# Performance work log

Measured on AMD Instinct MI355X. Metric: run time of the kernel, lower is better.

Reference implementation:

```python
import jax, jax.numpy as jnp
import numpy as np

H = 512
W = 512
SAMPLES = 32        # samples_per_segment hardcoded in render_filled_path
SIGMA = 1.0         # default anti-aliasing width
CHUNK = 32          # edges processed per scan step (mirrors torch chunk_size)


def setup_inputs() -> dict:
    key = jax.random.key(0)
    k1, k2 = jax.random.split(key)
    # 64 cubic segments -> 3*64+1 = 193 control points in image coordinates
    scale = jnp.array([W, H], dtype=jnp.float32)
    control_points = jax.random.uniform(k1, (193, 2), dtype=jnp.float32) * scale
    color = jax.random.uniform(k2, (3,), dtype=jnp.float32)
    return {"control_points": control_points, "color": color}


def _sample_bezier(cp):
    # cp: [3S+1, 2] -> sampled points [S*SAMPLES, 2]
    S = (cp.shape[0] - 1) // 3
    p0 = cp[0:3 * S:3][:, None, :]      # [S,1,2]
    p1 = cp[1:3 * S:3][:, None, :]
    p2 = cp[2:3 * S:3][:, None, :]
    p3 = cp[3:3 * S + 1:3][:, None, :]
    t = jnp.linspace(0.0, 1.0, SAMPLES, dtype=jnp.float32)[None, :, None]  # [1,T,1]
    mt = 1.0 - t
    pts = (mt ** 3) * p0 + 3.0 * (mt ** 2) * t * p1 + 3.0 * mt * (t ** 2) * p2 + (t ** 3) * p3
    return pts.reshape(-1, 2)  # [S*T, 2]


def _winding(path_points, sigma):
    # soft scanline winding number over HxW grid, edges (j, (j+1)%M)
    M = path_points.shape[0]
    p0 = path_points                      # [M,2]
    p1 = jnp.roll(path_points, -1, axis=0)
    gy = jnp.arange(H, dtype=jnp.float32)[:, None]   # [H,1]
    gx = jnp.arange(W, dtype=jnp.float32)[None, :]   # [1,W]
    # M = 64*32 = 2048 is divisible by CHUNK
    edges = jnp.stack([p0, p1], axis=1).reshape(M // CHUNK, CHUNK, 2, 2)

    def body(wind, ech):
        a, b = ech[:, 0], ech[:, 1]                       # [CHUNK,2]
        x0 = a[:, 0][:, None, None]; y0 = a[:, 1][:, None, None]
        x1 = b[:, 0][:, None, None]; y1 = b[:, 1][:, None, None]
        dy = y1 - y0                                      # [CHUNK,1,1]
        t_cross = (gy[None] - y0) / (dy + 1e-8)           # [CHUNK,H,1]
        x_cross = x0 + t_cross * (x1 - x0)                # [CHUNK,H,1]
        valid_t = jax.nn.sigmoid(t_cross * 20.0) * jax.nn.sigmoid((1.0 - t_cross) * 20.0)
        crosses = jax.nn.sigmoid((x_cross - gx[None]) / sigma)  # [CHUNK,H,W]
        mask = (jnp.abs(dy) >= 1e-6).astype(jnp.float32)  # skip degenerate edges
        contrib = crosses * (valid_t * jnp.sign(dy) * mask)
        return wind + jnp.sum(contrib, axis=0), None

    wind0 = jnp.zeros((H, W), dtype=jnp.float32)
    wind, _ = jax.lax.scan(body, wind0, edges)
    return wind


def reference(control_points, color):
    path = _sample_bezier(control_points)        # [2048,2]
    winding = _winding(path, SIGMA)              # [H,W]
    alpha = jax.nn.sigmoid(winding * 4.0)
    rgb = jnp.broadcast_to(color[None, None, :], (H, W, 3))
    return jnp.concatenate([rgb, alpha[..., None]], axis=-1)  # [H,W,4]
```

## Files before the change

### kernel.cpp

```cpp
#include <hip/hip_runtime.h>
#include <math.h>

#define HH 512
#define WW 512
#define M 2048
#define TPB 256
#define TWIN 18
#define WPIX 37
#define EPB 6

__device__ __forceinline__ float sigmoidf(float z) {
    return __builtin_amdgcn_rcpf(1.0f + __expf(-z));
}

__global__ __launch_bounds__(TPB) void bezier_render_kernel(
    const float* __restrict__ cp,
    const float* __restrict__ color,
    float* __restrict__ out)
{
    __shared__ float2 cps2[194];
    __shared__ float2 pts[M];
    __shared__ float  smoothv[WW];
    __shared__ float  cbin[WW + 1];
    __shared__ float  wtot[4];
    __shared__ float2 act[M];
    __shared__ int    nact;

    const int t    = threadIdx.x;
    const int lane = t & 63;
    const int wv   = t >> 6;
    const int y    = blockIdx.x;
    const float gy = (float)y;

    if (t < 193) cps2[t] = ((const float2*)cp)[t];
    if (t == 0) { nact = 0; cbin[WW] = 0.0f; }
    for (int x = t; x < WW; x += TPB) { smoothv[x] = 0.0f; cbin[x] = 0.0f; }
    __syncthreads();

    for (int m = t; m < M; m += TPB) {
        int s = m >> 5;
        int i = m & 31;
        float tt = (float)i * (1.0f / 31.0f);
        float mt = 1.0f - tt;
        float w0 = mt * mt * mt;
        float w1 = 3.0f * mt * mt * tt;
        float w2 = 3.0f * mt * tt * tt;
        float w3 = tt * tt * tt;
        float2 P0 = cps2[3 * s], P1 = cps2[3 * s + 1];
        float2 P2 = cps2[3 * s + 2], P3 = cps2[3 * s + 3];
        pts[m] = make_float2(w0 * P0.x + w1 * P1.x + w2 * P2.x + w3 * P3.x,
                             w0 * P0.y + w1 * P1.y + w2 * P2.y + w3 * P3.y);
    }
    __syncthreads();

    for (int e = t; e < M; e += TPB) {
        float2 a = pts[e];
        float2 b = pts[(e + 1) & (M - 1)];
        float dy = b.y - a.y;
        float tc = (gy - a.y) * __builtin_amdgcn_rcpf(dy + 1e-8f);
        if (!(fabsf(dy) >= 1e-6f) || !(tc > -0.8059f) || !(tc < 1.8059f)) continue;
        float ea = __expf(-20.0f * tc);
        float eb = __expf(-20.0f * (1.0f - tc));
        float v = __builtin_amdgcn_rcpf((1.0f + ea) * (1.0f + eb));
        float w = (dy > 0.0f) ? v : -v;
        float xc = fmaf(tc, b.x - a.x, a.x);
        int A = (int)floorf(xc) - TWIN;
        int bin = (A > WW) ? WW : A;
        if (bin > 0) atomicAdd(&cbin[bin], w);
        if (A < WW && A > -WPIX) {
            int idx = atomicAdd(&nact, 1);
            act[idx] = make_float2(xc, w);
        }
    }
    __syncthreads();

    {
        int na = nact;
        int el = t / WPIX;
        int k  = t - el * WPIX;
        if (el < EPB) {
            for (int e = el; e < na; e += EPB) {
                float2 xw = act[e];
                int x = (int)floorf(xw.x) - TWIN + k;
                if ((unsigned)x < (unsigned)WW) {
                    atomicAdd(&smoothv[x], xw.y * sigmoidf(xw.x - (float)x));
                }
            }
        }
    }
    __syncthreads();

    float e0 = cbin[2 * t];
    float e1 = cbin[2 * t + 1];
    float p  = e0 + e1;
    float v  = p;
#pragma unroll
    for (int off = 1; off < 64; off <<= 1) {
        float o = __shfl_down(v, off, 64);
        if (lane + off < 64) v += o;
    }
    if (lane == 0) wtot[wv] = v;
    __syncthreads();
    float hsum = 0.0f;
    if (wv < 1) hsum += wtot[1];
    if (wv < 2) hsum += wtot[2];
    if (wv < 3) hsum += wtot[3];
    float S    = v - p + hsum;
    float c512 = cbin[WW];
    float wc1  = S + c512;
    float wc0  = e1 + wc1;

    float r = color[0], g = color[1], bl = color[2];
    int x0 = 2 * t;
    float a0 = sigmoidf(4.0f * (wc0 + smoothv[x0]));
    float a1 = sigmoidf(4.0f * (wc1 + smoothv[x0 + 1]));
    float4* out4 = (float4*)out;
    out4[y * WW + x0]     = make_float4(r, g, bl, a0);
    out4[y * WW + x0 + 1] = make_float4(r, g, bl, a1);
}

extern "C" void kernel_launch(void* const* d_in, const int* in_sizes, int n_in,
                              void* d_out, int out_size, void* d_ws, size_t ws_size,
                              hipStream_t stream) {
    const float* cp    = (const float*)d_in[0];
    const float* color = (const float*)d_in[1];
    float* out = (float*)d_out;
    bezier_render_kernel<<<dim3(HH), dim3(TPB), 0, stream>>>(cp, color, out);
}
```

Measured before the change: 71.48 us.

## Bin edge crossings per row in a pre-pass instead of per-row full edge scan

Splits the single render kernel into three launches: a zeroing kernel, an edge-binning kernel and a render kernel. In the binning kernel one wavefront per edge computes the rows that edge can affect and appends (x-crossing, weight) records to per-row global lists using atomic counters. The render kernel then reads only its row's records instead of every block resampling the Bezier curve and testing all 2048 edges. The aim is to remove the redundant per-row sampling and edge tests. In exchange it adds two extra launches, global atomic traffic and a workspace round trip.

Result: slower. 77.78 us (+8.8%).

```diff
diff --git a/kernel.cpp b/kernel.cpp
--- a/kernel.cpp
+++ b/kernel.cpp
@@ -8,79 +8,114 @@
 #define TWIN 18
 #define WPIX 37
 #define EPB 6
+#define CAP 2048
+
 
 __device__ __forceinline__ float sigmoidf(float z) {
     return __builtin_amdgcn_rcpf(1.0f + __expf(-z));
 }
 
-__global__ __launch_bounds__(TPB) void bezier_render_kernel(
+__device__ __forceinline__ float2 sample_pt(const float2* __restrict__ cp2, int m) {
+    int s = m >> 5;
+    int i = m & 31;
+    float tt = (float)i * (1.0f / 31.0f);
+    float mt = 1.0f - tt;
+    float w0 = mt * mt * mt;
+    float w1 = 3.0f * mt * mt * tt;
+    float w2 = 3.0f * mt * tt * tt;
+    float w3 = tt * tt * tt;
+    float2 P0 = cp2[3 * s], P1 = cp2[3 * s + 1];
+    float2 P2 = cp2[3 * s + 2], P3 = cp2[3 * s + 3];
+    return make_float2(w0 * P0.x + w1 * P1.x + w2 * P2.x + w3 * P3.x,
+                       w0 * P0.y + w1 * P1.y + w2 * P2.y + w3 * P3.y);
+}
+
+__global__ __launch_bounds__(256) void zero_kernel(int* __restrict__ cnt) {
+    int t = threadIdx.x;
+    cnt[t] = 0;
+    cnt[t + 256] = 0;
+}
+
+__global__ __launch_bounds__(TPB) void bin_kernel(
     const float* __restrict__ cp,
-    const float* __restrict__ color,
+    int* __restrict__ cnt,
+    float2* __restrict__ rec)
+{
+    const int lane = threadIdx.x & 63;
+    const int e = (blockIdx.x << 2) + (threadIdx.x >> 6);
+
+    const float2* cp2 = (const float2*)cp;
+    float2 a = sample_pt(cp2, e);
+    float2 b = sample_pt(cp2, (e + 1) & (M - 1));
+
+    float dy = b.y - a.y;
+    if (!(fabsf(dy) >= 1e-6f)) return;
+
+    float d    = dy + 1e-8f;
+    float rcpd = __builtin_amdgcn_rcpf(d);
+
+    float g0 = fmaf(-0.8059f, d, a.y);
+    float g1 = fmaf( 1.8059f, d, a.y);
+    float lo = fminf(g0, g1), hi = fmaxf(g0, g1);
+    int r0 = (int)floorf(lo); if (r0 < 0)  r0 = 0;
+    int r1 = (int)ceilf(hi);  if (r1 > HH - 1) r1 = HH - 1;
+
+    float dx = b.x - a.x;
+    for (int r = r0 + lane; r <= r1; r += 64) {
+        float gy = (float)r;
+        float tc = (gy - a.y) * rcpd;
+        if (!(tc > -0.8059f) || !(tc < 1.8059f)) continue;
+        float ea = __expf(-20.0f * tc);
+        float eb = __expf(-20.0f * (1.0f - tc));
+        float v  = __builtin_amdgcn_rcpf((1.0f + ea) * (1.0f + eb));
+        float w  = (dy > 0.0f) ? v : -v;
+        float xc = fmaf(tc, dx, a.x);
+        int A = (int)floorf(xc) - TWIN;
+        if (A > -WPIX) {
+            int idx = atomicAdd(&cnt[r], 1);
+            if (idx < CAP) rec[(r << 11) + idx] = make_float2(xc, w);
+        }
+    }
+}
+
+__global__ __launch_bounds__(TPB) void render_kernel(
+    const int*    __restrict__ cnt,
+    const float2* __restrict__ rec,
+    const float*  __restrict__ color,
     float* __restrict__ out)
 {
-    __shared__ float2 cps2[194];
-    __shared__ float2 pts[M];
+    __shared__ float2 act[CAP];
     __shared__ float  smoothv[WW];
     __shared__ float  cbin[WW + 1];
     __shared__ float  wtot[4];
-    __shared__ float2 act[M];
-    __shared__ int    nact;
 
     const int t    = threadIdx.x;
     const int lane = t & 63;
     const int wv   = t >> 6;
     const int y    = blockIdx.x;
-    const float gy = (float)y;
 
-    if (t < 193) cps2[t] = ((const float2*)cp)[t];
-    if (t == 0) { nact = 0; cbin[WW] = 0.0f; }
+    int na = cnt[y];
+    if (na > CAP) na = CAP;
+
     for (int x = t; x < WW; x += TPB) { smoothv[x] = 0.0f; cbin[x] = 0.0f; }
+    if (t == 0) cbin[WW] = 0.0f;
     __syncthreads();
 
-    for (int m = t; m < M; m += TPB) {
-        int s = m >> 5;
-        int i = m & 31;
-        float tt = (float)i * (1.0f / 31.0f);
-        float mt = 1.0f - tt;
-        float w0 = mt * mt * mt;
-        float w1 = 3.0f * mt * mt * tt;
-        float w2 = 3.0f * mt * tt * tt;
-        float w3 = tt * tt * tt;
-        float2 P0 = cps2[3 * s], P1 = cps2[3 * s + 1];
-        float2 P2 = cps2[3 * s + 2], P3 = cps2[3 * s + 3];
-        pts[m] = make_float2(w0 * P0.x + w1 * P1.x + w2 * P2.x + w3 * P3.x,
-                             w0 * P0.y + w1 * P1.y + w2 * P2.y + w3 * P3.y);
-    }
-    __syncthreads();
-
-    for (int e = t; e < M; e += TPB) {
-        float2 a = pts[e];
-        float2 b = pts[(e + 1) & (M - 1)];
-        float dy = b.y - a.y;
-        float tc = (gy - a.y) * __builtin_amdgcn_rcpf(dy + 1e-8f);
-        if (!(fabsf(dy) >= 1e-6f) || !(tc > -0.8059f) || !(tc < 1.8059f)) continue;
-        float ea = __expf(-20.0f * tc);
-        float eb = __expf(-20.0f * (1.0f - tc));
-        float v = __builtin_amdgcn_rcpf((1.0f + ea) * (1.0f + eb));
-        float w = (dy > 0.0f) ? v : -v;
-        float xc = fmaf(tc, b.x - a.x, a.x);
-        int A = (int)floorf(xc) - TWIN;
+    for (int e2 = t; e2 < na; e2 += TPB) {
+        float2 xw = rec[(y << 11) + e2];
+        act[e2] = xw;
+        int A = (int)floorf(xw.x) - TWIN;
         int bin = (A > WW) ? WW : A;
-        if (bin > 0) atomicAdd(&cbin[bin], w);
-        if (A < WW && A > -WPIX) {
-            int idx = atomicAdd(&nact, 1);
-            act[idx] = make_float2(xc, w);
-        }
+        if (bin > 0) atomicAdd(&cbin[bin], xw.y);
     }
     __syncthreads();
 
     {
-        int na = nact;
         int el = t / WPIX;
         int k  = t - el * WPIX;
         if (el < EPB) {
-            for (int e = el; e < na; e += EPB) {
-                float2 xw = act[e];
+            for (int e2 = el; e2 < na; e2 += EPB) {
+                float2 xw = act[e2];
                 int x = (int)floorf(xw.x) - TWIN + k;
                 if ((unsigned)x < (unsigned)WW) {
                     atomicAdd(&smoothv[x], xw.y * sigmoidf(xw.x - (float)x));
@@ -125,5 +160,11 @@
     const float* cp    = (const float*)d_in[0];
     const float* color = (const float*)d_in[1];
     float* out = (float*)d_out;
-    bezier_render_kernel<<<dim3(HH), dim3(TPB), 0, stream>>>(cp, color, out);
+
+    int*    cnt = (int*)d_ws;
+    float2* rec = (float2*)((char*)d_ws + 4096);
+
+    zero_kernel  <<<dim3(1),     dim3(256), 0, stream>>>(cnt);
+    bin_kernel   <<<dim3(M / 4), dim3(TPB), 0, stream>>>(cp, cnt, rec);
+    render_kernel<<<dim3(HH),    dim3(TPB), 0, stream>>>(cnt, rec, color, out);
 }
```

## Process two rows per block to share Bezier sampling and edge setup

Applied to the files above, without the earlier changes.

Each block now handles two image rows with 512 threads instead of one row with 256. The Bezier sampling into shared memory and the per-edge setup (dy, reciprocal, dx) are computed once and reused for both rows, halving the redundant per-block sampling work. The cost is doubling shared memory for the per-row buffers and halving the grid to 256 blocks, which on a 256-CU device may reduce latency hiding and occupancy.

After: 77.67 us. +8.7%, slower.

```diff
diff --git a/kernel.cpp b/kernel.cpp
--- a/kernel.cpp
+++ b/kernel.cpp
@@ -4,7 +4,8 @@
 #define HH 512
 #define WW 512
 #define M 2048
-#define TPB 256
+#define TPB 512
+#define ROWS 2
 #define TWIN 18
 #define WPIX 37
 #define EPB 6
@@ -20,21 +21,23 @@
 {
     __shared__ float2 cps2[194];
     __shared__ float2 pts[M];
-    __shared__ float  smoothv[WW];
-    __shared__ float  cbin[WW + 1];
-    __shared__ float  wtot[4];
-    __shared__ float2 act[M];
-    __shared__ int    nact;
+    __shared__ float  smoothv[ROWS][WW];
+    __shared__ float  cbin[ROWS][WW + 1];
+    __shared__ float  wtot[ROWS][4];
+    __shared__ float2 act[ROWS][M];
+    __shared__ int    nact[ROWS];
 
     const int t    = threadIdx.x;
     const int lane = t & 63;
-    const int wv   = t >> 6;
-    const int y    = blockIdx.x;
-    const float gy = (float)y;
+    const int grp  = t >> 8;
+    const int tl   = t & 255;
+    const int wv   = tl >> 6;
+    const int y0   = blockIdx.x * ROWS;
 
     if (t < 193) cps2[t] = ((const float2*)cp)[t];
-    if (t == 0) { nact = 0; cbin[WW] = 0.0f; }
-    for (int x = t; x < WW; x += TPB) { smoothv[x] = 0.0f; cbin[x] = 0.0f; }
+    if (t < ROWS) { nact[t] = 0; cbin[t][WW] = 0.0f; }
+    for (int x = t; x < ROWS * WW; x += TPB) smoothv[x >> 9][x & (WW - 1)] = 0.0f;
+    for (int x = t; x < ROWS * WW; x += TPB) cbin[x >> 9][x & (WW - 1)] = 0.0f;
     __syncthreads();
 
     for (int m = t; m < M; m += TPB) {
@@ -57,41 +60,48 @@
         float2 a = pts[e];
         float2 b = pts[(e + 1) & (M - 1)];
         float dy = b.y - a.y;
-        float tc = (gy - a.y) * __builtin_amdgcn_rcpf(dy + 1e-8f);
-        if (!(fabsf(dy) >= 1e-6f) || !(tc > -0.8059f) || !(tc < 1.8059f)) continue;
-        float ea = __expf(-20.0f * tc);
-        float eb = __expf(-20.0f * (1.0f - tc));
-        float v = __builtin_amdgcn_rcpf((1.0f + ea) * (1.0f + eb));
-        float w = (dy > 0.0f) ? v : -v;
-        float xc = fmaf(tc, b.x - a.x, a.x);
-        int A = (int)floorf(xc) - TWIN;
-        int bin = (A > WW) ? WW : A;
-        if (bin > 0) atomicAdd(&cbin[bin], w);
-        if (A < WW && A > -WPIX) {
-            int idx = atomicAdd(&nact, 1);
-            act[idx] = make_float2(xc, w);
+        if (!(fabsf(dy) >= 1e-6f)) continue;
+        float rcpd = __builtin_amdgcn_rcpf(dy + 1e-8f);
+        float dx = b.x - a.x;
+#pragma unroll
+        for (int rr = 0; rr < ROWS; ++rr) {
+            float gy = (float)(y0 + rr);
+            float tc = (gy - a.y) * rcpd;
+            if (!(tc > -0.8059f) || !(tc < 1.8059f)) continue;
+            float ea = __expf(-20.0f * tc);
+            float eb = __expf(-20.0f * (1.0f - tc));
+            float v = __builtin_amdgcn_rcpf((1.0f + ea) * (1.0f + eb));
+            float w = (dy > 0.0f) ? v : -v;
+            float xc = fmaf(tc, dx, a.x);
+            int A = (int)floorf(xc) - TWIN;
+            int bin = (A > WW) ? WW : A;
+            if (bin > 0) atomicAdd(&cbin[rr][bin], w);
+            if (A < WW && A > -WPIX) {
+                int idx = atomicAdd(&nact[rr], 1);
+                act[rr][idx] = make_float2(xc, w);
+            }
         }
     }
     __syncthreads();
 
     {
-        int na = nact;
-        int el = t / WPIX;
-        int k  = t - el * WPIX;
+        int na = nact[grp];
+        int el = tl / WPIX;
+        int k  = tl - el * WPIX;
         if (el < EPB) {
             for (int e = el; e < na; e += EPB) {
-                float2 xw = act[e];
+                float2 xw = act[grp][e];
                 int x = (int)floorf(xw.x) - TWIN + k;
                 if ((unsigned)x < (unsigned)WW) {
-                    atomicAdd(&smoothv[x], xw.y * sigmoidf(xw.x - (float)x));
+                    atomicAdd(&smoothv[grp][x], xw.y * sigmoidf(xw.x - (float)x));
                 }
             }
         }
     }
     __syncthreads();
 
-    float e0 = cbin[2 * t];
-    float e1 = cbin[2 * t + 1];
+    float e0 = cbin[grp][2 * tl];
+    float e1 = cbin[grp][2 * tl + 1];
     float p  = e0 + e1;
     float v  = p;
 #pragma unroll
@@ -99,21 +109,22 @@
         float o = __shfl_down(v, off, 64);
         if (lane + off < 64) v += o;
     }
-    if (lane == 0) wtot[wv] = v;
+    if (lane == 0) wtot[grp][wv] = v;
     __syncthreads();
     float hsum = 0.0f;
-    if (wv < 1) hsum += wtot[1];
-    if (wv < 2) hsum += wtot[2];
-    if (wv < 3) hsum += wtot[3];
+    if (wv < 1) hsum += wtot[grp][1];
+    if (wv < 2) hsum += wtot[grp][2];
+    if (wv < 3) hsum += wtot[grp][3];
     float S    = v - p + hsum;
-    float c512 = cbin[WW];
+    float c512 = cbin[grp][WW];
     float wc1  = S + c512;
     float wc0  = e1 + wc1;
 
     float r = color[0], g = color[1], bl = color[2];
-    int x0 = 2 * t;
-    float a0 = sigmoidf(4.0f * (wc0 + smoothv[x0]));
-    float a1 = sigmoidf(4.0f * (wc1 + smoothv[x0 + 1]));
+    int x0 = 2 * tl;
+    int y  = y0 + grp;
+    float a0 = sigmoidf(4.0f * (wc0 + smoothv[grp][x0]));
+    float a1 = sigmoidf(4.0f * (wc1 + smoothv[grp][x0 + 1]));
     float4* out4 = (float4*)out;
     out4[y * WW + x0]     = make_float4(r, g, bl, a0);
     out4[y * WW + x0 + 1] = make_float4(r, g, bl, a1);
@@ -125,5 +136,5 @@
     const float* cp    = (const float*)d_in[0];
     const float* color = (const float*)d_in[1];
     float* out = (float*)d_out;
-    bezier_render_kernel<<<dim3(HH), dim3(TPB), 0, stream>>>(cp, color, out);
+    bezier_render_kernel<<<dim3(HH / ROWS), dim3(TPB), 0, stream>>>(cp, color, out);
 }
```
